# Kernel optimization log

Hardware: AMD Instinct MI355X
Metric: run time of the kernel (lower is better)

Reference implementation:

```python
import jax, jax.numpy as jnp
import numpy as np

N_HEAD = 16

def setup_inputs() -> dict:
    key = jax.random.key(0)
    k0, k1, k2, k3 = jax.random.split(key, 4)
    S, E, H, T = 2048, 1024, N_HEAD, 4096
    d = E // H
    return {
        "x": jax.random.normal(k0, (S, E), jnp.float32),
        "past": jax.random.normal(k1, (2, H, T, d), jnp.float32),  # stacked [pk, pv]
        "W1": jax.random.normal(k2, (E, 3 * E), jnp.float32) * 0.02,  # c_attn (Conv1D k=1 == linear)
        "b1": jnp.zeros((3 * E,), jnp.float32),
        "W2": jax.random.normal(k3, (E, E), jnp.float32) * 0.02,  # c_proj
        "b2": jnp.zeros((E,), jnp.float32),
        "past_length": 2048,
    }


def reference(x, past, W1, b1, W2, b2, past_length):
    H = N_HEAD
    S, E = x.shape
    d = E // H

    c = x @ W1 + b1  # [S, 3E]
    q, k, v = jnp.split(c, 3, axis=1)

    def split_heads(t):  # [S, E] -> [H, S, d]
        return jnp.transpose(t.reshape(S, H, d), (1, 0, 2))

    q, k, v = split_heads(q), split_heads(k), split_heads(v)

    pk, pv = past[0], past[1]  # [H, T, d]
    k = jax.lax.dynamic_update_slice_in_dim(pk, k, past_length, axis=1)
    v = jax.lax.dynamic_update_slice_in_dim(pv, v, past_length, axis=1)

    # attention scores [H, S, T]
    w = jnp.einsum('hid,hjd->hij', q, k) / np.sqrt(d)
    ns = k.shape[1]
    i = jnp.arange(S)[:, None]
    j = jnp.arange(ns)[None, :]
    b = (i >= j - past_length).astype(w.dtype)
    w = w * b - jnp.float32(1e10) * (1 - b)
    w = jax.nn.softmax(w, axis=-1)

    a = jnp.einsum('hij,hjd->hid', w, v)  # [H, S, d]
    # faithful to original: start index clamps to 0 since axis len == S
    a = jax.lax.dynamic_slice_in_dim(a, past_length, S, axis=1)
    a = jnp.transpose(a, (1, 0, 2)).reshape(S, E)  # merge heads

    out = a @ W2 + b2
    new_cache = jnp.stack([k, v], axis=0)
    return out, new_cache
```

## Files before the change

### kernel.cpp

```cpp
#include <hip/hip_runtime.h>
#include <hip/hip_bf16.h>
#include <stdint.h>


#define S_LEN 2048
#define E_DIM 1024
#define NHEAD 16
#define HDIM  64
#define T_LEN 4096
#define PASTL 2048

typedef __bf16 bf16x8 __attribute__((ext_vector_type(8)));
typedef __bf16 bf16x4 __attribute__((ext_vector_type(4)));
typedef float  f32x4  __attribute__((ext_vector_type(4)));

static __device__ __forceinline__ f32x4 mfma_bf16(bf16x8 a, bf16x8 b, f32x4 c) {
  return __builtin_amdgcn_mfma_f32_16x16x32_bf16(a, b, c, 0, 0, 0);
}

static __device__ __forceinline__ unsigned short f2bf(float f) {
  union { float f; unsigned int u; } v; v.f = f;
  unsigned int u = v.u;
  return (unsigned short)((u + 0x7fffu + ((u >> 16) & 1u)) >> 16);
}

static __device__ __forceinline__ float bf2f(unsigned short u) {
  union { unsigned int u; float f; } v; v.u = (unsigned int)u << 16;
  return v.f;
}

#define GLOBAL_LOAD_LDS16(gptr, lptr)                                              \
  __builtin_amdgcn_global_load_lds(                                                \
      (const __attribute__((address_space(1))) unsigned int*)(gptr),               \
      (__attribute__((address_space(3))) unsigned int*)(lptr), 16, 0, 0)


__global__ void copy_past_kernel(const float* __restrict__ past,
                                 float* __restrict__ cache,
                                 unsigned short* __restrict__ kb) {
  const int n4 = (2 * NHEAD * PASTL * HDIM) / 4;
  for (int i = blockIdx.x * blockDim.x + threadIdx.x; i < n4;
       i += gridDim.x * blockDim.x) {
    int e = i * 4;
    int d = e & 63;
    int t = (e >> 6) & (PASTL - 1);
    int hh = (e >> 17) & (NHEAD - 1);
    int kv = e >> 21;
    size_t full = (((size_t)kv * NHEAD + hh) * T_LEN + t) * HDIM + d;
    float4 v = *(const float4*)(past + full);
    *(float4*)(cache + full) = v;
    if (kv == 0) {
      ushort4 u;
      u.x = f2bf(v.x); u.y = f2bf(v.y); u.z = f2bf(v.z); u.w = f2bf(v.w);
      *(ushort4*)(kb + full) = u;
    }
  }
}

__global__ void convert_kernel(const float* __restrict__ in,
                               unsigned short* __restrict__ out, int n4) {
  for (int i = blockIdx.x * blockDim.x + threadIdx.x; i < n4;
       i += gridDim.x * blockDim.x) {
    float4 v = ((const float4*)in)[i];
    ushort4 u;
    u.x = f2bf(v.x); u.y = f2bf(v.y); u.z = f2bf(v.z); u.w = f2bf(v.w);
    ((ushort4*)out)[i] = u;
  }
}

__global__ void transpose_convert_kernel(const float* __restrict__ in,
                                         unsigned short* __restrict__ out,
                                         int rows, int cols) {
  __shared__ float tile[64][65];
  const int c0 = blockIdx.x * 64, r0 = blockIdx.y * 64;
  const int tx = threadIdx.x & 63, ty = threadIdx.x >> 6;
#pragma unroll
  for (int r = 0; r < 64; r += 4)
    tile[r + ty][tx] = in[(size_t)(r0 + r + ty) * cols + c0 + tx];
  __syncthreads();
#pragma unroll
  for (int r = 0; r < 64; r += 4)
    out[(size_t)(c0 + r + ty) * rows + r0 + tx] = f2bf(tile[tx][r + ty]);
}

__global__ void vtrans_kernel(const float* __restrict__ vin,
                              unsigned short* __restrict__ vt) {
  __shared__ float tile[64][65];
  const int h = blockIdx.y;
  const int t0 = blockIdx.x * 64;
  const float* in = vin + (size_t)h * T_LEN * HDIM;
  unsigned short* out = vt + (size_t)h * HDIM * T_LEN;
  const int tx = threadIdx.x & 63, ty = threadIdx.x >> 6;
#pragma unroll
  for (int r = 0; r < 64; r += 4)
    tile[r + ty][tx] = in[(size_t)(t0 + r + ty) * HDIM + tx];
  __syncthreads();
#pragma unroll
  for (int r = 0; r < 64; r += 4)
    out[(size_t)(r + ty) * T_LEN + t0 + tx] = f2bf(tile[tx][r + ty]);
}

template <int MODE>
__global__ __launch_bounds__(256) void gemm_bt_kernel(
    const unsigned short* __restrict__ A, const unsigned short* __restrict__ Bt,
    const float* __restrict__ bias, int K,
    float* __restrict__ out_f32, unsigned short* __restrict__ qb,
    float* __restrict__ cache_k, float* __restrict__ cache_v,
    unsigned short* __restrict__ kb) {
  __shared__ alignas(16) unsigned short As[128 * 64];
  __shared__ alignas(16) unsigned short Bs[128 * 64];
  const int tid = threadIdx.x;
  const int lane = tid & 63;
  const int w = tid >> 6;
  const int wm = w >> 1, wn = w & 1;
  const int m0 = blockIdx.y * 128, n0 = blockIdx.x * 128;

  f32x4 acc[4][4];
#pragma unroll
  for (int i = 0; i < 4; ++i)
#pragma unroll
    for (int j = 0; j < 4; ++j) acc[i][j] = f32x4{0.f, 0.f, 0.f, 0.f};

  const int rbase = w * 8 + (lane >> 3);
  const int sbase = lane & 7;

  for (int k0 = 0; k0 < K; k0 += 64) {
#pragma unroll
    for (int q = 0; q < 4; ++q) {
      int row_l = q * 32 + rbase;
      int slot = sbase ^ (row_l & 7);
      const unsigned short* ga = A + (size_t)(m0 + row_l) * K + k0 + slot * 8;
      const unsigned short* gb = Bt + (size_t)(n0 + row_l) * K + k0 + slot * 8;
      unsigned int ldsOff = (unsigned int)(q * 4096 + w * 1024);
      GLOBAL_LOAD_LDS16(ga, (char*)As + ldsOff);
      GLOBAL_LOAD_LDS16(gb, (char*)Bs + ldsOff);
    }
    __syncthreads();
#pragma unroll
    for (int kk = 0; kk < 2; ++kk) {
      bf16x8 af[4], bfr[4];
#pragma unroll
      for (int mi = 0; mi < 4; ++mi) {
        int row = wm * 64 + mi * 16 + (lane & 15);
        int slot = (kk * 4 + (lane >> 4)) ^ (row & 7);
        af[mi] = *reinterpret_cast<const bf16x8*>((const char*)As + row * 128 + slot * 16);
      }
#pragma unroll
      for (int ni = 0; ni < 4; ++ni) {
        int row = wn * 64 + ni * 16 + (lane & 15);
        int slot = (kk * 4 + (lane >> 4)) ^ (row & 7);
        bfr[ni] = *reinterpret_cast<const bf16x8*>((const char*)Bs + row * 128 + slot * 16);
      }
#pragma unroll
      for (int mi = 0; mi < 4; ++mi)
#pragma unroll
        for (int ni = 0; ni < 4; ++ni)
          acc[mi][ni] = mfma_bf16(af[mi], bfr[ni], acc[mi][ni]);
    }
    __syncthreads();
  }

#pragma unroll
  for (int ni = 0; ni < 4; ++ni) {
    int n = n0 + wn * 64 + ni * 16 + (lane & 15);
    float bv = bias[n];
#pragma unroll
    for (int mi = 0; mi < 4; ++mi) {
#pragma unroll
      for (int r = 0; r < 4; ++r) {
        int m = m0 + wm * 64 + mi * 16 + (lane >> 4) * 4 + r;
        float val = acc[mi][ni][r] + bv;
        if (MODE == 0) {
          if (n < E_DIM) {
            qb[(size_t)m * E_DIM + n] = f2bf(val * 0.18033688f);
          } else if (n < 2 * E_DIM) {
            int e = n - E_DIM;
            size_t idx = ((size_t)(e >> 6) * T_LEN + (PASTL + m)) * HDIM + (e & 63);
            cache_k[idx] = val;
            kb[idx] = f2bf(val);
          } else {
            int e = n - 2 * E_DIM;
            size_t idx = ((size_t)(e >> 6) * T_LEN + (PASTL + m)) * HDIM + (e & 63);
            cache_v[idx] = val;
          }
        } else {
          out_f32[(size_t)m * E_DIM + n] = val;
        }
      }
    }
  }
}

__global__ __launch_bounds__(256) void attn_kernel(
    const unsigned short* __restrict__ qb, const unsigned short* __restrict__ kb,
    const unsigned short* __restrict__ vt,
    unsigned short* __restrict__ o_part, float* __restrict__ l_part) {
  __shared__ alignas(16) unsigned short Ks[2][64 * 64];
  __shared__ alignas(16) unsigned short Vs[2][64 * 64];
  __shared__ alignas(16) __bf16 p_lds[4][32][72];
  const int fid = blockIdx.x;
  const int h = (fid & 7) + ((fid >= 448) ? 8 : 0);
  const int g = (fid >> 3) - ((fid >= 448) ? 56 : 0);
  int x, c;
  if (g < 24) { x = g / 3; c = g - 3 * x; }
  else { int g2 = g - 24; x = 8 + (g2 >> 2); c = g2 & 3; }

  const int tid = threadIdx.x;
  const int w = tid >> 6;
  const int lane = tid & 63;
  const int lr = lane & 15;
  const int lg = lane >> 4;
  const int qb0 = x * 128;
  const int q0 = qb0 + w * 32;

  const unsigned short* qr0 = qb + (size_t)(q0 + lr) * E_DIM + h * HDIM + lg * 8;
  const unsigned short* qr1 = qb + (size_t)(q0 + 16 + lr) * E_DIM + h * HDIM + lg * 8;
  const bf16x8 qf00 = *reinterpret_cast<const bf16x8*>(qr0);
  const bf16x8 qf01 = *reinterpret_cast<const bf16x8*>(qr0 + 32);
  const bf16x8 qf10 = *reinterpret_cast<const bf16x8*>(qr1);
  const bf16x8 qf11 = *reinterpret_cast<const bf16x8*>(qr1 + 32);

  const unsigned short* kh = kb + (size_t)h * T_LEN * HDIM;
  const unsigned short* vh = vt + (size_t)h * HDIM * T_LEN;

  const int srow = tid >> 3;
  const int sseg = (tid & 7) ^ (srow & 7);
  const unsigned short* ksrc = kh + (size_t)srow * HDIM + sseg * 8;
  const unsigned short* vsrc = vh + (size_t)srow * T_LEN + sseg * 8;

  f32x4 o[2][4];
  float lsum[2][2];
#pragma unroll
  for (int sb = 0; sb < 2; ++sb) {
    lsum[sb][0] = lsum[sb][1] = 0.f;
#pragma unroll
    for (int jd = 0; jd < 4; ++jd) o[sb][jd] = f32x4{0.f, 0.f, 0.f, 0.f};
  }

  const int jmaxq = q0 + PASTL;
  const int NTfull = 34 + 2 * x;
  const int tb = c * 16;
  const int te = (tb + 16 < NTfull) ? tb + 16 : NTfull;
  const int tbeg = tb * 64, tend = te * 64;

  auto stage = [&](int b, int t0) {
    GLOBAL_LOAD_LDS16(ksrc + (size_t)t0 * HDIM, (char*)Ks[b] + tid * 16);
    GLOBAL_LOAD_LDS16(ksrc + (size_t)(t0 + 32) * HDIM, (char*)Ks[b] + 4096 + tid * 16);
    GLOBAL_LOAD_LDS16(vsrc + t0, (char*)Vs[b] + tid * 16);
    GLOBAL_LOAD_LDS16(vsrc + t0 + (size_t)32 * T_LEN, (char*)Vs[b] + 4096 + tid * 16);
  };

  stage(0, tbeg);
  int cur = 0;
  for (int t0 = tbeg; t0 < tend; t0 += 64) {
    asm volatile("s_waitcnt vmcnt(0)" ::: "memory");
    __syncthreads();
    if (t0 + 64 < tend) stage(cur ^ 1, t0 + 64);

    bf16x8 kf[4][2];
#pragma unroll
    for (int j = 0; j < 4; ++j) {
      int row = j * 16 + lr;
      int s0 = lg ^ (row & 7), s1 = (4 + lg) ^ (row & 7);
      kf[j][0] = *reinterpret_cast<const bf16x8*>((const char*)Ks[cur] + row * 128 + s0 * 16);
      kf[j][1] = *reinterpret_cast<const bf16x8*>((const char*)Ks[cur] + row * 128 + s1 * 16);
    }

    f32x4 sc[2][4];
#pragma unroll
    for (int sb = 0; sb < 2; ++sb)
#pragma unroll
      for (int j = 0; j < 4; ++j) sc[sb][j] = f32x4{0.f, 0.f, 0.f, 0.f};
    __builtin_amdgcn_s_setprio(1);
#pragma unroll
    for (int j = 0; j < 4; ++j) {
      sc[0][j] = mfma_bf16(kf[j][0], qf00, sc[0][j]);
      sc[0][j] = mfma_bf16(kf[j][1], qf01, sc[0][j]);
      sc[1][j] = mfma_bf16(kf[j][0], qf10, sc[1][j]);
      sc[1][j] = mfma_bf16(kf[j][1], qf11, sc[1][j]);
    }
    __builtin_amdgcn_s_setprio(0);

    const bool partial = (t0 + 63 > jmaxq);
    const int thr = q0 + PASTL - t0 + lr;
    const int lg4 = lg * 4;
#pragma unroll
    for (int sb = 0; sb < 2; ++sb) {
#pragma unroll
      for (int j = 0; j < 4; ++j) {
        bf16x4 pk;
#pragma unroll
        for (int r = 0; r < 4; ++r) {
          float p = __builtin_amdgcn_exp2f(sc[sb][j][r]);
          if (partial && (j * 16 + lg4 + r > thr + sb * 16)) p = 0.f;
          lsum[sb][r >> 1] += p;
          pk[r] = (__bf16)p;
        }
        *reinterpret_cast<bf16x4*>(&p_lds[w][sb * 16 + lr][j * 16 + lg4]) = pk;
      }
    }

    bf16x8 pa[2][2];
#pragma unroll
    for (int sb = 0; sb < 2; ++sb) {
      pa[sb][0] = *reinterpret_cast<const bf16x8*>(&p_lds[w][sb * 16 + lr][lg * 8]);
      pa[sb][1] = *reinterpret_cast<const bf16x8*>(&p_lds[w][sb * 16 + lr][32 + lg * 8]);
    }
    __builtin_amdgcn_s_setprio(1);
#pragma unroll
    for (int jd = 0; jd < 4; ++jd) {
      int row = jd * 16 + lr;
      int s0 = lg ^ (row & 7), s1 = (4 + lg) ^ (row & 7);
      bf16x8 vf0 = *reinterpret_cast<const bf16x8*>((const char*)Vs[cur] + row * 128 + s0 * 16);
      bf16x8 vf1 = *reinterpret_cast<const bf16x8*>((const char*)Vs[cur] + row * 128 + s1 * 16);
      o[0][jd] = mfma_bf16(pa[0][0], vf0, o[0][jd]);
      o[0][jd] = mfma_bf16(pa[0][1], vf1, o[0][jd]);
      o[1][jd] = mfma_bf16(pa[1][0], vf0, o[1][jd]);
      o[1][jd] = mfma_bf16(pa[1][1], vf1, o[1][jd]);
    }
    __builtin_amdgcn_s_setprio(0);
    cur ^= 1;
  }

  unsigned short* op = o_part + ((size_t)(c * NHEAD + h) * S_LEN) * HDIM;
  float* lp = l_part + (size_t)(c * NHEAD + h) * S_LEN;
#pragma unroll
  for (int sb = 0; sb < 2; ++sb) {
    float ls = lsum[sb][0] + lsum[sb][1];
    ls += __shfl_xor(ls, 16);
    ls += __shfl_xor(ls, 32);
    if (lg == 0) lp[q0 + sb * 16 + lr] = ls;
#pragma unroll
    for (int jd = 0; jd < 4; ++jd) {
#pragma unroll
      for (int r = 0; r < 4; ++r) {
        int row = q0 + sb * 16 + lg * 4 + r;
        op[(size_t)row * HDIM + jd * 16 + lr] = f2bf(o[sb][jd][r]);
      }
    }
  }
}

__global__ __launch_bounds__(256) void attn_merge_kernel(
    const unsigned short* __restrict__ o_part, const float* __restrict__ l_part,
    unsigned short* __restrict__ ab) {
  const int flat = blockIdx.x * 256 + threadIdx.x;
  const int d4 = flat & 15;
  const int row = (flat >> 4) & (S_LEN - 1);
  const int h = flat >> 15;
  const int nc = (row < 1024) ? 3 : 4;
  const size_t cstride_o = (size_t)NHEAD * S_LEN * HDIM;
  const size_t base_o = (((size_t)h * S_LEN) + row) * HDIM + d4 * 4;
  float acc[4] = {0.f, 0.f, 0.f, 0.f};
  float l = 0.f;
  for (int cc = 0; cc < nc; ++cc) {
    ushort4 u = *(const ushort4*)(o_part + cc * cstride_o + base_o);
    acc[0] += bf2f(u.x); acc[1] += bf2f(u.y);
    acc[2] += bf2f(u.z); acc[3] += bf2f(u.w);
    l += l_part[(size_t)cc * NHEAD * S_LEN + (size_t)h * S_LEN + row];
  }
  float inv = 1.f / l;
  ushort4 u;
  u.x = f2bf(acc[0] * inv);
  u.y = f2bf(acc[1] * inv);
  u.z = f2bf(acc[2] * inv);
  u.w = f2bf(acc[3] * inv);
  *(ushort4*)(ab + (size_t)row * E_DIM + h * HDIM + d4 * 4) = u;
}


extern "C" void kernel_launch(void* const* d_in, const int* in_sizes, int n_in,
                              void* d_out, int out_size, void* d_ws, size_t ws_size,
                              hipStream_t stream) {
  (void)in_sizes; (void)n_in; (void)out_size; (void)ws_size;
  const float* x    = (const float*)d_in[0];
  const float* past = (const float*)d_in[1];
  const float* W1   = (const float*)d_in[2];
  const float* b1   = (const float*)d_in[3];
  const float* W2   = (const float*)d_in[4];
  const float* b2   = (const float*)d_in[5];

  float* out = (float*)d_out;
  float* cache_k = out + (size_t)S_LEN * E_DIM;
  float* cache_v = cache_k + (size_t)NHEAD * T_LEN * HDIM;

  char* ws = (char*)d_ws;
  unsigned short* xb  = (unsigned short*)(ws);
  unsigned short* ab  = (unsigned short*)(ws);
  unsigned short* w1t = (unsigned short*)(ws + (size_t)(4u  << 20));
  unsigned short* vt  = (unsigned short*)(ws + (size_t)(4u  << 20));
  unsigned short* w2t = (unsigned short*)(ws + (size_t)(12u << 20));
  unsigned short* qb  = (unsigned short*)(ws + (size_t)(14u << 20));
  unsigned short* kb  = (unsigned short*)(ws + (size_t)(18u << 20));
  unsigned short* o_part = (unsigned short*)(ws + (size_t)(26u << 20));
  float* l_part = (float*)(ws + (size_t)(42u << 20));

  copy_past_kernel<<<2048, 256, 0, stream>>>(past, cache_k, kb);
  convert_kernel<<<1024, 256, 0, stream>>>(x, xb, (S_LEN * E_DIM) / 4);
  transpose_convert_kernel<<<dim3(3072 / 64, 1024 / 64), 256, 0, stream>>>(W1, w1t, 1024, 3072);
  transpose_convert_kernel<<<dim3(1024 / 64, 1024 / 64), 256, 0, stream>>>(W2, w2t, 1024, 1024);
  gemm_bt_kernel<0><<<dim3(3072 / 128, 2048 / 128), 256, 0, stream>>>(
      xb, w1t, b1, 1024, nullptr, qb, cache_k, cache_v, kb);
  vtrans_kernel<<<dim3(T_LEN / 64, NHEAD), 256, 0, stream>>>(cache_v, vt);
  attn_kernel<<<dim3(896), 256, 0, stream>>>(qb, kb, vt, o_part, l_part);
  attn_merge_kernel<<<(NHEAD * S_LEN * 16) / 256, 256, 0, stream>>>(o_part, l_part, ab);
  gemm_bt_kernel<1><<<dim3(1024 / 128, 2048 / 128), 256, 0, stream>>>(
      ab, w2t, b2, 1024, out, nullptr, nullptr, nullptr, nullptr);
}
```

Before: 135.6 us.

## Switch attention to 32x32x16 MFMA and pass P through registers via lane shuffles

Rewrites the attention inner loop to use 32x32x16 bf16 MFMA tiles instead of 16x16x32, computing transposed scores so each lane holds a column of P. The probability tile is packed to bf16 in registers and redistributed with cross-half shuffles to form the A operand of the PV product, which removes the per-wave p_lds shared-memory round trip. Launch bounds request 4 blocks per SM. The larger tiles mean fewer MFMA issues and LDS reads, at the cost of more accumulator registers and a manual bf16 rounding step.

```diff
diff --git a/kernel.cpp b/kernel.cpp
--- a/kernel.cpp
+++ b/kernel.cpp
@@ -11,17 +11,20 @@
 #define PASTL 2048
 
 typedef __bf16 bf16x8 __attribute__((ext_vector_type(8)));
-typedef __bf16 bf16x4 __attribute__((ext_vector_type(4)));
 typedef float  f32x4  __attribute__((ext_vector_type(4)));
+typedef float  f32x16 __attribute__((ext_vector_type(16)));
 
 static __device__ __forceinline__ f32x4 mfma_bf16(bf16x8 a, bf16x8 b, f32x4 c) {
   return __builtin_amdgcn_mfma_f32_16x16x32_bf16(a, b, c, 0, 0, 0);
 }
-
-static __device__ __forceinline__ unsigned short f2bf(float f) {
+static __device__ __forceinline__ f32x16 mfma32(bf16x8 a, bf16x8 b, f32x16 c) {
+  return __builtin_amdgcn_mfma_f32_32x32x16_bf16(a, b, c, 0, 0, 0);
+}
+
+static __device__ __forceinline__ unsigned int f2bf(float f) {
   union { float f; unsigned int u; } v; v.f = f;
   unsigned int u = v.u;
-  return (unsigned short)((u + 0x7fffu + ((u >> 16) & 1u)) >> 16);
+  return (u + 0x7fffu + ((u >> 16) & 1u)) >> 16;
 }
 
 static __device__ __forceinline__ float bf2f(unsigned short u) {
@@ -191,13 +194,12 @@
   }
 }
 
-__global__ __launch_bounds__(256) void attn_kernel(
+__global__ __launch_bounds__(256, 4) void attn_kernel(
     const unsigned short* __restrict__ qb, const unsigned short* __restrict__ kb,
     const unsigned short* __restrict__ vt,
     unsigned short* __restrict__ o_part, float* __restrict__ l_part) {
   __shared__ alignas(16) unsigned short Ks[2][64 * 64];
   __shared__ alignas(16) unsigned short Vs[2][64 * 64];
-  __shared__ alignas(16) __bf16 p_lds[4][32][72];
   const int fid = blockIdx.x;
   const int h = (fid & 7) + ((fid >= 448) ? 8 : 0);
   const int g = (fid >> 3) - ((fid >= 448) ? 56 : 0);
@@ -208,17 +210,16 @@
   const int tid = threadIdx.x;
   const int w = tid >> 6;
   const int lane = tid & 63;
-  const int lr = lane & 15;
-  const int lg = lane >> 4;
-  const int qb0 = x * 128;
-  const int q0 = qb0 + w * 32;
-
-  const unsigned short* qr0 = qb + (size_t)(q0 + lr) * E_DIM + h * HDIM + lg * 8;
-  const unsigned short* qr1 = qb + (size_t)(q0 + 16 + lr) * E_DIM + h * HDIM + lg * 8;
-  const bf16x8 qf00 = *reinterpret_cast<const bf16x8*>(qr0);
-  const bf16x8 qf01 = *reinterpret_cast<const bf16x8*>(qr0 + 32);
-  const bf16x8 qf10 = *reinterpret_cast<const bf16x8*>(qr1);
-  const bf16x8 qf11 = *reinterpret_cast<const bf16x8*>(qr1 + 32);
+  const int l31 = lane & 31;
+  const int hi = lane >> 5;
+  const int hi4 = hi * 4;
+  const int q0 = x * 128 + w * 32;
+
+  const unsigned short* qrow = qb + (size_t)(q0 + l31) * E_DIM + h * HDIM + hi * 8;
+  bf16x8 qf[4];
+#pragma unroll
+  for (int kk = 0; kk < 4; ++kk)
+    qf[kk] = *reinterpret_cast<const bf16x8*>(qrow + kk * 16);
 
   const unsigned short* kh = kb + (size_t)h * T_LEN * HDIM;
   const unsigned short* vh = vt + (size_t)h * HDIM * T_LEN;
@@ -228,20 +229,16 @@
   const unsigned short* ksrc = kh + (size_t)srow * HDIM + sseg * 8;
   const unsigned short* vsrc = vh + (size_t)srow * T_LEN + sseg * 8;
 
-  f32x4 o[2][4];
-  float lsum[2][2];
-#pragma unroll
-  for (int sb = 0; sb < 2; ++sb) {
-    lsum[sb][0] = lsum[sb][1] = 0.f;
-#pragma unroll
-    for (int jd = 0; jd < 4; ++jd) o[sb][jd] = f32x4{0.f, 0.f, 0.f, 0.f};
-  }
-
-  const int jmaxq = q0 + PASTL;
+  f32x16 o0, o1;
+#pragma unroll
+  for (int i = 0; i < 16; ++i) { o0[i] = 0.f; o1[i] = 0.f; }
+  float lsum = 0.f;
+
   const int NTfull = 34 + 2 * x;
   const int tb = c * 16;
   const int te = (tb + 16 < NTfull) ? tb + 16 : NTfull;
   const int tbeg = tb * 64, tend = te * 64;
+  const int qpp = q0 + l31 + PASTL;
 
   auto stage = [&](int b, int t0) {
     GLOBAL_LOAD_LDS16(ksrc + (size_t)t0 * HDIM, (char*)Ks[b] + tid * 16);
@@ -257,87 +254,93 @@
     __syncthreads();
     if (t0 + 64 < tend) stage(cur ^ 1, t0 + 64);
 
-    bf16x8 kf[4][2];
-#pragma unroll
-    for (int j = 0; j < 4; ++j) {
-      int row = j * 16 + lr;
-      int s0 = lg ^ (row & 7), s1 = (4 + lg) ^ (row & 7);
-      kf[j][0] = *reinterpret_cast<const bf16x8*>((const char*)Ks[cur] + row * 128 + s0 * 16);
-      kf[j][1] = *reinterpret_cast<const bf16x8*>((const char*)Ks[cur] + row * 128 + s1 * 16);
-    }
-
-    f32x4 sc[2][4];
-#pragma unroll
-    for (int sb = 0; sb < 2; ++sb)
-#pragma unroll
-      for (int j = 0; j < 4; ++j) sc[sb][j] = f32x4{0.f, 0.f, 0.f, 0.f};
+    f32x16 s0, s1;
+#pragma unroll
+    for (int i = 0; i < 16; ++i) { s0[i] = 0.f; s1[i] = 0.f; }
     __builtin_amdgcn_s_setprio(1);
 #pragma unroll
-    for (int j = 0; j < 4; ++j) {
-      sc[0][j] = mfma_bf16(kf[j][0], qf00, sc[0][j]);
-      sc[0][j] = mfma_bf16(kf[j][1], qf01, sc[0][j]);
-      sc[1][j] = mfma_bf16(kf[j][0], qf10, sc[1][j]);
-      sc[1][j] = mfma_bf16(kf[j][1], qf11, sc[1][j]);
+    for (int kk = 0; kk < 4; ++kk) {
+      int row0 = l31, row1 = 32 + l31;
+      int sl0 = (kk * 2 + hi) ^ (row0 & 7);
+      int sl1 = (kk * 2 + hi) ^ (row1 & 7);
+      bf16x8 kf0 = *reinterpret_cast<const bf16x8*>((const char*)Ks[cur] + row0 * 128 + sl0 * 16);
+      bf16x8 kf1 = *reinterpret_cast<const bf16x8*>((const char*)Ks[cur] + row1 * 128 + sl1 * 16);
+      s0 = mfma32(kf0, qf[kk], s0);
+      s1 = mfma32(kf1, qf[kk], s1);
     }
     __builtin_amdgcn_s_setprio(0);
 
-    const bool partial = (t0 + 63 > jmaxq);
-    const int thr = q0 + PASTL - t0 + lr;
-    const int lg4 = lg * 4;
-#pragma unroll
-    for (int sb = 0; sb < 2; ++sb) {
-#pragma unroll
-      for (int j = 0; j < 4; ++j) {
-        bf16x4 pk;
-#pragma unroll
-        for (int r = 0; r < 4; ++r) {
-          float p = __builtin_amdgcn_exp2f(sc[sb][j][r]);
-          if (partial && (j * 16 + lg4 + r > thr + sb * 16)) p = 0.f;
-          lsum[sb][r >> 1] += p;
-          pk[r] = (__bf16)p;
-        }
-        *reinterpret_cast<bf16x4*>(&p_lds[w][sb * 16 + lr][j * 16 + lg4]) = pk;
+    bf16x8 vf0[4], vf1[4];
+#pragma unroll
+    for (int ks = 0; ks < 4; ++ks) {
+      int row0 = l31, row1 = 32 + l31;
+      int sl0 = (ks * 2 + hi) ^ (row0 & 7);
+      int sl1 = (ks * 2 + hi) ^ (row1 & 7);
+      vf0[ks] = *reinterpret_cast<const bf16x8*>((const char*)Vs[cur] + row0 * 128 + sl0 * 16);
+      vf1[ks] = *reinterpret_cast<const bf16x8*>((const char*)Vs[cur] + row1 * 128 + sl1 * 16);
+    }
+
+    const bool partial = (t0 + 63 > q0 + PASTL);
+    const int thr = qpp - t0;
+    unsigned int dw0[8], dw1[8];
+#pragma unroll
+    for (int i = 0; i < 8; ++i) {
+      int r0 = 2 * i;
+      int ko = (r0 & 3) + 8 * (r0 >> 2) + hi4;
+      float p0 = __builtin_amdgcn_exp2f(s0[r0]);
+      float p1 = __builtin_amdgcn_exp2f(s0[r0 + 1]);
+      float p2 = __builtin_amdgcn_exp2f(s1[r0]);
+      float p3 = __builtin_amdgcn_exp2f(s1[r0 + 1]);
+      if (partial) {
+        if (ko > thr) p0 = 0.f;
+        if (ko + 1 > thr) p1 = 0.f;
+        if (ko + 32 > thr) p2 = 0.f;
+        if (ko + 33 > thr) p3 = 0.f;
       }
-    }
-
-    bf16x8 pa[2][2];
-#pragma unroll
-    for (int sb = 0; sb < 2; ++sb) {
-      pa[sb][0] = *reinterpret_cast<const bf16x8*>(&p_lds[w][sb * 16 + lr][lg * 8]);
-      pa[sb][1] = *reinterpret_cast<const bf16x8*>(&p_lds[w][sb * 16 + lr][32 + lg * 8]);
-    }
+      lsum += (p0 + p1) + (p2 + p3);
+      dw0[i] = (f2bf(p1) << 16) | f2bf(p0);
+      dw1[i] = (f2bf(p3) << 16) | f2bf(p2);
+    }
+
+    bf16x8 pa[4];
+#pragma unroll
+    for (int ks = 0; ks < 4; ++ks) {
+      const unsigned int* dwp = (ks < 2) ? dw0 : dw1;
+      int base = 4 * (ks & 1);
+      unsigned int lo0 = dwp[base + 0], lo1 = dwp[base + 1];
+      unsigned int hi0 = dwp[base + 2], hi1 = dwp[base + 3];
+      unsigned int s_0 = hi ? lo0 : hi0;
+      unsigned int s_1 = hi ? lo1 : hi1;
+      unsigned int r_0 = __shfl_xor((int)s_0, 32);
+      unsigned int r_1 = __shfl_xor((int)s_1, 32);
+      union { unsigned int u[4]; bf16x8 v; } pu;
+      pu.u[0] = hi ? r_0 : lo0;
+      pu.u[1] = hi ? r_1 : lo1;
+      pu.u[2] = hi ? hi0 : r_0;
+      pu.u[3] = hi ? hi1 : r_1;
+      pa[ks] = pu.v;
+    }
+
     __builtin_amdgcn_s_setprio(1);
 #pragma unroll
-    for (int jd = 0; jd < 4; ++jd) {
-      int row = jd * 16 + lr;
-      int s0 = lg ^ (row & 7), s1 = (4 + lg) ^ (row & 7);
-      bf16x8 vf0 = *reinterpret_cast<const bf16x8*>((const char*)Vs[cur] + row * 128 + s0 * 16);
-      bf16x8 vf1 = *reinterpret_cast<const bf16x8*>((const char*)Vs[cur] + row * 128 + s1 * 16);
-      o[0][jd] = mfma_bf16(pa[0][0], vf0, o[0][jd]);
-      o[0][jd] = mfma_bf16(pa[0][1], vf1, o[0][jd]);
-      o[1][jd] = mfma_bf16(pa[1][0], vf0, o[1][jd]);
-      o[1][jd] = mfma_bf16(pa[1][1], vf1, o[1][jd]);
+    for (int ks = 0; ks < 4; ++ks) {
+      o0 = mfma32(pa[ks], vf0[ks], o0);
+      o1 = mfma32(pa[ks], vf1[ks], o1);
     }
     __builtin_amdgcn_s_setprio(0);
     cur ^= 1;
   }
 
+  lsum += __shfl_xor(lsum, 32);
+
   unsigned short* op = o_part + ((size_t)(c * NHEAD + h) * S_LEN) * HDIM;
   float* lp = l_part + (size_t)(c * NHEAD + h) * S_LEN;
-#pragma unroll
-  for (int sb = 0; sb < 2; ++sb) {
-    float ls = lsum[sb][0] + lsum[sb][1];
-    ls += __shfl_xor(ls, 16);
-    ls += __shfl_xor(ls, 32);
-    if (lg == 0) lp[q0 + sb * 16 + lr] = ls;
-#pragma unroll
-    for (int jd = 0; jd < 4; ++jd) {
-#pragma unroll
-      for (int r = 0; r < 4; ++r) {
-        int row = q0 + sb * 16 + lg * 4 + r;
-        op[(size_t)row * HDIM + jd * 16 + lr] = f2bf(o[sb][jd][r]);
-      }
-    }
+  if (hi == 0) lp[q0 + l31] = lsum;
+#pragma unroll
+  for (int r = 0; r < 16; ++r) {
+    int qr = (r & 3) + 8 * (r >> 2) + hi4;
+    op[(size_t)(q0 + qr) * HDIM + l31] = f2bf(o0[r]);
+    op[(size_t)(q0 + qr) * HDIM + 32 + l31] = f2bf(o1[r]);
   }
 }
 
```

Result: no change. 136.8 us (+0.8%).

## Split K/V staging in attention loop and fuse prep conversion kernels

Applied to the files above, without the earlier changes.

The attention loop now stages K and V tiles separately, with two barriers per iteration. Each wait uses vmcnt(2) instead of waiting for all loads, so the next tile's V load can be in flight during the QK and softmax work while the next K load overlaps the PV work. The copy_past and x-conversion kernels are merged into a single prep launch to save one kernel launch. The finer-grained pipelining adds a second barrier per tile and relies on the vmcnt counts being correct for the order in which loads are issued.

```diff
diff --git a/kernel.cpp b/kernel.cpp
--- a/kernel.cpp
+++ b/kernel.cpp
@@ -18,10 +18,10 @@
   return __builtin_amdgcn_mfma_f32_16x16x32_bf16(a, b, c, 0, 0, 0);
 }
 
-static __device__ __forceinline__ unsigned short f2bf(float f) {
+static __device__ __forceinline__ unsigned int f2bf(float f) {
   union { float f; unsigned int u; } v; v.f = f;
   unsigned int u = v.u;
-  return (unsigned short)((u + 0x7fffu + ((u >> 16) & 1u)) >> 16);
+  return (u + 0x7fffu + ((u >> 16) & 1u)) >> 16;
 }
 
 static __device__ __forceinline__ float bf2f(unsigned short u) {
@@ -35,36 +35,36 @@
       (__attribute__((address_space(3))) unsigned int*)(lptr), 16, 0, 0)
 
 
-__global__ void copy_past_kernel(const float* __restrict__ past,
-                                 float* __restrict__ cache,
-                                 unsigned short* __restrict__ kb) {
-  const int n4 = (2 * NHEAD * PASTL * HDIM) / 4;
-  for (int i = blockIdx.x * blockDim.x + threadIdx.x; i < n4;
+__global__ void prep_kernel(const float* __restrict__ past,
+                            const float* __restrict__ x,
+                            float* __restrict__ cache,
+                            unsigned short* __restrict__ kb,
+                            unsigned short* __restrict__ xb) {
+  const int n4p = (2 * NHEAD * PASTL * HDIM) / 4;
+  const int n4x = (S_LEN * E_DIM) / 4;
+  for (int i = blockIdx.x * blockDim.x + threadIdx.x; i < n4p + n4x;
        i += gridDim.x * blockDim.x) {
-    int e = i * 4;
-    int d = e & 63;
-    int t = (e >> 6) & (PASTL - 1);
-    int hh = (e >> 17) & (NHEAD - 1);
-    int kv = e >> 21;
-    size_t full = (((size_t)kv * NHEAD + hh) * T_LEN + t) * HDIM + d;
-    float4 v = *(const float4*)(past + full);
-    *(float4*)(cache + full) = v;
-    if (kv == 0) {
+    if (i < n4p) {
+      int e = i * 4;
+      int d = e & 63;
+      int t = (e >> 6) & (PASTL - 1);
+      int hh = (e >> 17) & (NHEAD - 1);
+      int kv = e >> 21;
+      size_t full = (((size_t)kv * NHEAD + hh) * T_LEN + t) * HDIM + d;
+      float4 v = *(const float4*)(past + full);
+      *(float4*)(cache + full) = v;
+      if (kv == 0) {
+        ushort4 u;
+        u.x = f2bf(v.x); u.y = f2bf(v.y); u.z = f2bf(v.z); u.w = f2bf(v.w);
+        *(ushort4*)(kb + full) = u;
+      }
+    } else {
+      int j = i - n4p;
+      float4 v = ((const float4*)x)[j];
       ushort4 u;
       u.x = f2bf(v.x); u.y = f2bf(v.y); u.z = f2bf(v.z); u.w = f2bf(v.w);
-      *(ushort4*)(kb + full) = u;
-    }
-  }
-}
-
-__global__ void convert_kernel(const float* __restrict__ in,
-                               unsigned short* __restrict__ out, int n4) {
-  for (int i = blockIdx.x * blockDim.x + threadIdx.x; i < n4;
-       i += gridDim.x * blockDim.x) {
-    float4 v = ((const float4*)in)[i];
-    ushort4 u;
-    u.x = f2bf(v.x); u.y = f2bf(v.y); u.z = f2bf(v.z); u.w = f2bf(v.w);
-    ((ushort4*)out)[i] = u;
+      ((ushort4*)xb)[j] = u;
+    }
   }
 }
 
@@ -241,21 +241,28 @@
   const int NTfull = 34 + 2 * x;
   const int tb = c * 16;
   const int te = (tb + 16 < NTfull) ? tb + 16 : NTfull;
-  const int tbeg = tb * 64, tend = te * 64;
-
-  auto stage = [&](int b, int t0) {
+  const int NT = te - tb;
+  const int tbeg = tb * 64;
+
+  auto stageK = [&](int b, int t0) {
     GLOBAL_LOAD_LDS16(ksrc + (size_t)t0 * HDIM, (char*)Ks[b] + tid * 16);
     GLOBAL_LOAD_LDS16(ksrc + (size_t)(t0 + 32) * HDIM, (char*)Ks[b] + 4096 + tid * 16);
+  };
+  auto stageV = [&](int b, int t0) {
     GLOBAL_LOAD_LDS16(vsrc + t0, (char*)Vs[b] + tid * 16);
     GLOBAL_LOAD_LDS16(vsrc + t0 + (size_t)32 * T_LEN, (char*)Vs[b] + 4096 + tid * 16);
   };
 
-  stage(0, tbeg);
+  stageK(0, tbeg);
+  stageV(0, tbeg);
   int cur = 0;
-  for (int t0 = tbeg; t0 < tend; t0 += 64) {
-    asm volatile("s_waitcnt vmcnt(0)" ::: "memory");
-    __syncthreads();
-    if (t0 + 64 < tend) stage(cur ^ 1, t0 + 64);
+  int t0 = tbeg;
+  for (int i = 0; i < NT; ++i, t0 += 64) {
+    const bool more = (i + 1 < NT);
+    asm volatile("s_waitcnt vmcnt(2)" ::: "memory");
+    __builtin_amdgcn_s_barrier();
+    __builtin_amdgcn_sched_barrier(0);
+    if (more) stageK(cur ^ 1, t0 + 64);
 
     bf16x8 kf[4][2];
 #pragma unroll
@@ -299,13 +306,22 @@
         *reinterpret_cast<bf16x4*>(&p_lds[w][sb * 16 + lr][j * 16 + lg4]) = pk;
       }
     }
-
     bf16x8 pa[2][2];
 #pragma unroll
     for (int sb = 0; sb < 2; ++sb) {
       pa[sb][0] = *reinterpret_cast<const bf16x8*>(&p_lds[w][sb * 16 + lr][lg * 8]);
       pa[sb][1] = *reinterpret_cast<const bf16x8*>(&p_lds[w][sb * 16 + lr][32 + lg * 8]);
     }
+
+    if (more) {
+      asm volatile("s_waitcnt vmcnt(2)" ::: "memory");
+    } else {
+      asm volatile("s_waitcnt vmcnt(0)" ::: "memory");
+    }
+    __builtin_amdgcn_s_barrier();
+    __builtin_amdgcn_sched_barrier(0);
+    if (more) stageV(cur ^ 1, t0 + 64);
+
     __builtin_amdgcn_s_setprio(1);
 #pragma unroll
     for (int jd = 0; jd < 4; ++jd) {
@@ -395,8 +411,7 @@
   unsigned short* o_part = (unsigned short*)(ws + (size_t)(26u << 20));
   float* l_part = (float*)(ws + (size_t)(42u << 20));
 
-  copy_past_kernel<<<2048, 256, 0, stream>>>(past, cache_k, kb);
-  convert_kernel<<<1024, 256, 0, stream>>>(x, xb, (S_LEN * E_DIM) / 4);
+  prep_kernel<<<2048, 256, 0, stream>>>(past, x, cache_k, kb, xb);
   transpose_convert_kernel<<<dim3(3072 / 64, 1024 / 64), 256, 0, stream>>>(W1, w1t, 1024, 3072);
   transpose_convert_kernel<<<dim3(1024 / 64, 1024 / 64), 256, 0, stream>>>(W2, w2t, 1024, 1024);
   gemm_bt_kernel<0><<<dim3(3072 / 128, 2048 / 128), 256, 0, stream>>>(
```

Result: no change. 136.2 us (+0.4%).
